# Optimization experiments

Measured on AMD Instinct MI355X. Metric: run time of the kernel, lower is better.

## Reference

```python
import jax, jax.numpy as jnp
import numpy as np

P = 7          # corr_size (patch size)
PAD = P // 2   # displacement radius
PP = P * P     # 49 correlation channels
CHANS = [512, 1024, 512, 256, 256, 256]
HW = [64, 32, 16, 8, 4, 2]
B = 8


def _spatial_correlation(f1, f2):
    """out[b, pi*P+pj, y, x] = sum_c f1[b,c,y,x] * f2[b,c,y+pi-PAD, x+pj-PAD] (zero pad)."""
    Bb, C, H, W = f1.shape
    f2p = jnp.pad(f2, ((0, 0), (0, 0), (PAD, PAD), (PAD, PAD)))
    outs = [jnp.sum(f1 * f2p[:, :, di:di + H, dj:dj + W], axis=1)
            for di in range(P) for dj in range(P)]
    return jnp.stack(outs, axis=1)  # [B, P*P, H, W]


def _corr_lstm_cell(feat, feat_pre, h_pre, c_pre, w, b):
    corr = jax.nn.leaky_relu(_spatial_correlation(feat, feat_pre), 0.01)  # [B,49,H,W]
    lstm_in = jnp.concatenate([corr, h_pre], axis=1)                      # [B,98,H,W]
    conv = jax.lax.conv_general_dilated(
        lstm_in, w, window_strides=(1, 1), padding='SAME',
        dimension_numbers=('NCHW', 'OIHW', 'NCHW')) + b[None, :, None, None]
    cc_i, cc_f, cc_o, cc_g = jnp.split(conv, 4, axis=1)
    i = jax.nn.sigmoid(cc_i)
    f = jax.nn.sigmoid(cc_f)
    o = jax.nn.sigmoid(cc_o)
    g = jnp.tanh(cc_g)
    c_next = f * c_pre + i * g
    h_next = o * jnp.tanh(c_next)
    return h_next, c_next, corr


def setup_inputs() -> dict:
    key = jax.random.key(0)
    ks = jax.random.split(key, 6 * 6)
    d = {}
    ki = 0
    for l in range(6):
        C, S = CHANS[l], HW[l]
        d[f'x{l}'] = 0.05 * jax.random.normal(ks[ki], (B, C, S, S), jnp.float32); ki += 1
        d[f'xp{l}'] = 0.05 * jax.random.normal(ks[ki], (B, C, S, S), jnp.float32); ki += 1
        d[f'h{l}'] = 0.1 * jax.random.normal(ks[ki], (B, PP, S, S), jnp.float32); ki += 1
        d[f'c{l}'] = 0.1 * jax.random.normal(ks[ki], (B, PP, S, S), jnp.float32); ki += 1
        fan_in = 2 * PP * 9
        lim = float(np.sqrt(6.0 / (fan_in + 4 * PP * 9)))
        d[f'w{l}'] = jax.random.uniform(ks[ki], (4 * PP, 2 * PP, 3, 3), jnp.float32, -lim, lim); ki += 1
        bias = jnp.zeros((4 * PP,), jnp.float32).at[PP:2 * PP].set(1.0)  # forget-gate bias = 1
        d[f'b{l}'] = bias; ki += 1
    return d


def reference(x0, x1, x2, x3, x4, x5,
              xp0, xp1, xp2, xp3, xp4, xp5,
              h0, h1, h2, h3, h4, h5,
              c0, c1, c2, c3, c4, c5,
              w0, w1, w2, w3, w4, w5,
              b0, b1, b2, b3, b4, b5):
    xs = [x0, x1, x2, x3, x4, x5]
    xps = [xp0, xp1, xp2, xp3, xp4, xp5]
    hs = [h0, h1, h2, h3, h4, h5]
    cs = [c0, c1, c2, c3, c4, c5]
    ws = [w0, w1, w2, w3, w4, w5]
    bs = [b0, b1, b2, b3, b4, b5]
    outs = []
    for l in range(6):
        outs.append(_corr_lstm_cell(xs[l], xps[l], hs[l], cs[l], ws[l], bs[l]))
    h_next = tuple(o[0] for o in outs)
    c_next = tuple(o[1] for o in outs)
    corrs = tuple(o[2] for o in outs)
    return h_next + c_next + corrs  # flat 18-tuple
```

## Files before the change

### kernel.cpp

```cpp
#include <hip/hip_runtime.h>
#include <stdint.h>

#define DEV __device__ __forceinline__

typedef _Float16 half2_t __attribute__((ext_vector_type(2)));
typedef _Float16 half4_t __attribute__((ext_vector_type(4)));
typedef __bf16   bf16x8  __attribute__((ext_vector_type(8)));
typedef float    floatx4 __attribute__((ext_vector_type(4)));
typedef float    floatx2 __attribute__((ext_vector_type(2)));

DEV float fdot2f(half2_t a, half2_t b, float c) {
#if __has_builtin(__builtin_amdgcn_fdot2)
  return __builtin_amdgcn_fdot2(a, b, c, false);
#else
  return c + (float)a[0] * (float)b[0] + (float)a[1] * (float)b[1];
#endif
}

DEV uint32_t f2bf(float f) {
  uint32_t u = __float_as_uint(f);
  return (u + 0x7FFFu + ((u >> 16) & 1u)) >> 16;
}

DEV half2_t mkh2(float a, float b) {
  half2_t r; r[0] = (_Float16)a; r[1] = (_Float16)b; return r;
}

struct CorrCfg {
  const float* gx[6]; const float* gxp[6];
  int wg_start[3];
  int small_start[3];
  int S[3], C[3], tiles_x[3], tiles_pb[3], cpl[3];
  int sS[3], sC[3];
  long long poff[3], spoff[3];
};

template<int TH, int TWD>
__global__ __launch_bounds__(128)
void corr_kernel(CorrCfg cfg, float* __restrict__ partial)
{
  int wg = blockIdx.x;
  if (wg >= cfg.small_start[0]) {
    int lvl = (wg >= cfg.small_start[2]) ? 2 : (wg >= cfg.small_start[1]) ? 1 : 0;
    long long i = (long long)(wg - cfg.small_start[lvl])*128 + threadIdx.x;
    const int S = cfg.sS[lvl], C = cfg.sC[lvl], SS = S*S;
    if (i >= (long long)8*49*SS) return;
    const float* X  = cfg.gx[lvl+3];
    const float* XP = cfg.gxp[lvl+3];
    int xc_ = (int)(i % S); int yc = (int)((i/S) % S);
    int d = (int)((i/SS) % 49); int b = (int)(i/((long long)49*SS));
    int yy = yc + d/7 - 3, xx = xc_ + (d%7) - 3;
    float s = 0.f;
    if (yy >= 0 && yy < S && xx >= 0 && xx < S) {
      const float* xb = X  + (size_t)b*C*SS + (size_t)yc*S + xc_;
      const float* pb = XP + (size_t)b*C*SS + (size_t)yy*S + xx;
      #pragma unroll 4
      for (int c = 0; c < C; ++c) s += xb[(size_t)c*SS] * pb[(size_t)c*SS];
    }
    partial[cfg.spoff[lvl] + i] = s;
    return;
  }
  constexpr int NT  = 128;
  constexpr int HWC = TWD + 6;
  constexpr int ST  = TWD + 10;
  constexpr int NPOS = (TH+6)*HWC;
  constexpr int PER  = (NPOS + NT - 1)/NT;
  __shared__ half2_t ldsbuf[2][2][(TH+6)*ST] __attribute__((aligned(16)));

  int lvl = (wg >= cfg.wg_start[2]) ? 2 : (wg >= cfg.wg_start[1]) ? 1 : 0;
  wg -= cfg.wg_start[lvl];
  const float* X  = cfg.gx[lvl];
  const float* XP = cfg.gxp[lvl];
  const int S = cfg.S[lvl], C = cfg.C[lvl];
  const int txc = cfg.tiles_x[lvl], tpb = cfg.tiles_pb[lvl], cpl = cfg.cpl[lvl];
  const int per_split = 8 * tpb;
  const int sp = wg / per_split;
  const int rem = wg - sp*per_split;
  const int b = rem / tpb;
  const int t = rem - b*tpb;
  const int y0 = (t / txc) * TH, x0t = (t % txc) * TWD;
  const int tid = threadIdx.x;
  const int tx = tid & (TWD/2 - 1), ty = tid / (TWD/2);
  const int cbase = sp * cpl;
  const size_t SS = (size_t)S*S;
  const float* Xb  = X  + (size_t)b*C*SS;
  const float* XPb = XP + (size_t)b*C*SS;
  const int py = y0 + ty, px = x0t + 2*tx;
  const size_t qoff = (size_t)py*S + px;

  int  f_lds[PER]; int f_go[PER]; bool f_ok[PER], f_val[PER];
  #pragma unroll
  for (int s = 0; s < PER; ++s) {
    int i = tid + s*NT;
    int r = i / HWC, c = i - r*HWC;
    int gy = y0 + r - 3, gx = x0t + c - 3;
    bool val = (i < NPOS);
    bool ok = val && gy >= 0 && gy < S && gx >= 0 && gx < S;
    f_val[s] = val; f_ok[s] = ok;
    f_go[s] = ok ? gy*S + gx : 0;
    f_lds[s] = val ? r*ST + c : 0;
  }

  floatx2 acc[49];
  #pragma unroll
  for (int d = 0; d < 49; ++d) acc[d] = (floatx2)0.0f;

  float fl[2][PER][2];
  float xc[4][2], xn[4][2];

#define FILL_LOAD(c0v) { \
  _Pragma("unroll") for (int pr = 0; pr < 2; ++pr) { \
    const float* p0_ = XPb + (size_t)(cbase + (c0v) + 2*pr)*SS; \
    const float* p1_ = p0_ + SS; \
    _Pragma("unroll") for (int s = 0; s < PER; ++s) { \
      fl[pr][s][0] = f_ok[s] ? p0_[f_go[s]] : 0.f; \
      fl[pr][s][1] = f_ok[s] ? p1_[f_go[s]] : 0.f; } } }

#define XLOAD(dst, c0v) { \
  _Pragma("unroll") for (int c = 0; c < 4; ++c) { \
    const float* q_ = Xb + (size_t)(cbase + (c0v) + c)*SS + qoff; \
    dst[c][0] = q_[0]; dst[c][1] = q_[1]; } }

#define FILL_STORE(bbv) { \
  _Pragma("unroll") for (int pr = 0; pr < 2; ++pr) \
    _Pragma("unroll") for (int s = 0; s < PER; ++s) \
      if (f_val[s]) ldsbuf[bbv][pr][f_lds[s]] = mkh2(fl[pr][s][0], fl[pr][s][1]); }

#define COMPUTE(bbv) { \
  _Pragma("unroll") for (int pr = 0; pr < 2; ++pr) { \
    half2_t xq0 = mkh2(xc[2*pr][0], xc[2*pr+1][0]); \
    half2_t xq1 = mkh2(xc[2*pr][1], xc[2*pr+1][1]); \
    _Pragma("unroll") for (int di = 0; di < 7; ++di) { \
      const half2_t* row_ = &ldsbuf[bbv][pr][(ty+di)*ST + 2*tx]; \
      half2_t w_[8]; \
      _Pragma("unroll") for (int k = 0; k < 4; ++k) { \
        half4_t v_ = *(const half4_t*)(row_ + 2*k); \
        w_[2*k]   = __builtin_shufflevector(v_, v_, 0, 1); \
        w_[2*k+1] = __builtin_shufflevector(v_, v_, 2, 3); } \
      _Pragma("unroll") for (int dj = 0; dj < 7; ++dj) { \
        acc[di*7+dj].x = fdot2f(xq0, w_[dj],   acc[di*7+dj].x); \
        acc[di*7+dj].y = fdot2f(xq1, w_[dj+1], acc[di*7+dj].y); } } } }

  const int nchunk = cpl >> 2;
  FILL_LOAD(0); XLOAD(xc, 0);
  FILL_STORE(0);
  FILL_LOAD(4); XLOAD(xn, 4);
  __syncthreads();
  for (int k = 0; k < nchunk; ++k) {
    const int bb = k & 1;
    if (k+1 < nchunk) FILL_STORE(bb^1);
    if (k+2 < nchunk) FILL_LOAD((k+2)*4);
    COMPUTE(bb);
    #pragma unroll
    for (int c = 0; c < 4; ++c) { xc[c][0] = xn[c][0]; xc[c][1] = xn[c][1]; }
    if (k+2 < nchunk) XLOAD(xn, (k+2)*4);
    __syncthreads();
  }
#undef FILL_LOAD
#undef XLOAD
#undef FILL_STORE
#undef COMPUTE

  float* P = partial + cfg.poff[lvl] + ((size_t)sp*8 + b)*49*SS + qoff;
  #pragma unroll
  for (int d = 0; d < 49; ++d)
    *(floatx2*)(P + (size_t)d*SS) = acc[d];
}

__global__ __launch_bounds__(256)
void pack_w_kernel(const float* __restrict__ w0, const float* __restrict__ w1,
                   const float* __restrict__ w2, const float* __restrict__ w3,
                   const float* __restrict__ w4, const float* __restrict__ w5,
                   uint16_t* __restrict__ wpack)
{
  int idx = blockIdx.x*256 + threadIdx.x;
  int lvl = idx / 258048;
  int e = idx - lvl*258048;
  const float* W = lvl==0?w0:lvl==1?w1:lvl==2?w2:lvl==3?w3:lvl==4?w4:w5;
  int j = e & 7, lane = (e >> 3) & 63, rest = e >> 9;
  int s = rest % 36, tt = rest / 36;
  int n  = tt*16 + (lane & 15);
  int ch = (s & 3)*32 + (lane >> 4)*8 + j;
  int tap = s >> 2, ky = tap/3, kx = tap - 3*ky;
  float v = 0.f;
  if (n < 196 && ch < 98) v = W[((n*98 + ch)*3 + ky)*3 + kx];
  wpack[idx] = (uint16_t)f2bf(v);
}

struct P2Cfg {
  int blk_start[7];
  int S[6], nsplit[6];
  long long poff[6], lstm_off[6], corr_off[6];
  const float* h[6];
};
__global__ __launch_bounds__(256)
void pass2_kernel(P2Cfg cfg, const float* __restrict__ partial,
                  uint16_t* __restrict__ lstm, float* __restrict__ dout)
{
  int blk = blockIdx.x;
  int lvl = 0;
  while (lvl < 5 && blk >= cfg.blk_start[lvl+1]) ++lvl;
  long long i = (long long)(blk - cfg.blk_start[lvl])*256 + threadIdx.x;
  const int S = cfg.S[lvl], Sp = S + 2, SS = S*S;
  if (i >= (long long)8*98*SS) return;
  int pix = (int)(i % SS);
  int ch  = (int)((i / SS) % 98);
  int b   = (int)(i / ((long long)98*SS));
  float val;
  if (ch < 49) {
    const int nsp = cfg.nsplit[lvl];
    const float* P = partial + cfg.poff[lvl] + ((size_t)b*49 + ch)*SS + pix;
    const size_t spstride = (size_t)8*49*SS;
    float s = 0.f;
    for (int sp = 0; sp < nsp; ++sp) s += P[(size_t)sp*spstride];
    s = s < 0.f ? 0.01f*s : s;
    dout[cfg.corr_off[lvl] + ((size_t)b*49 + ch)*SS + pix] = s;
    val = s;
  } else {
    val = cfg.h[lvl][((size_t)b*49 + (ch - 49))*SS + pix];
  }
  int y = pix / S, x = pix - y*S;
  lstm[cfg.lstm_off[lvl] + ((size_t)(b*Sp + y + 1)*Sp + (x + 1))*128 + ch] =
      (uint16_t)f2bf(val);
}

struct CCfg {
  int wg_start[7];
  int S[6], tiles_x[6], tiles_pb[6], lwsh[6], mfc[6], mgrp[6];
  long long lstm_off[6], wp_off[6], conv_off[6];
};
__global__ __launch_bounds__(256)
void conv_kernel(CCfg cfg, const uint16_t* __restrict__ lstm,
                 const uint16_t* __restrict__ wpack, float* __restrict__ cout)
{
  int wg = blockIdx.x;
  int lvl = 0;
  while (lvl < 5 && wg >= cfg.wg_start[lvl+1]) ++lvl;
  wg -= cfg.wg_start[lvl];
  const int S = cfg.S[lvl], Sp = S + 2;
  const int lwsh = cfg.lwsh[lvl], msk = (1 << lwsh) - 1;
  const int tpb = cfg.tiles_pb[lvl];
  const int b = wg / tpb, t = wg - b*tpb;
  const int ty0 = (t / cfg.tiles_x[lvl]) << (6 - lwsh);
  const int tx0 = (t % cfg.tiles_x[lvl]) << lwsh;
  const int wave = threadIdx.x >> 6, lane = threadIdx.x & 63;
  const int nhalf = wave & 1, mhalf = wave >> 1;
  const int mfc = cfg.mfc[lvl];
  if (mhalf >= cfg.mgrp[lvl]) return;
  const int mi = lane & 15, q = lane >> 4;
  const int SS = S*S;
  const uint16_t* lb = lstm + cfg.lstm_off[lvl] + (size_t)b*Sp*Sp*128;
  int aoff[2];
  #pragma unroll
  for (int mf = 0; mf < 2; ++mf) {
    int p = mhalf*32 + mf*16 + mi;
    int pc = p < SS ? p : 0;
    int y = ty0 + (pc >> lwsh), xx = tx0 + (pc & msk);
    aoff[mf] = (y*Sp + xx)*128 + q*8;
  }
  const uint16_t* wb = wpack + cfg.wp_off[lvl]
                     + (size_t)(nhalf*7)*36*512 + (size_t)lane*8;
  floatx4 acc[2][7];
  #pragma unroll
  for (int mf = 0; mf < 2; ++mf)
    #pragma unroll
    for (int nt = 0; nt < 7; ++nt) acc[mf][nt] = (floatx4)0.0f;

#define CONV_LOAD(sv, AV, BV) { \
  int tap_ = (sv) >> 2, cs_ = (sv) & 3; \
  int ky_ = tap_ / 3, kx_ = tap_ - 3*ky_; \
  int ao_ = ((ky_*Sp + kx_) << 7) + (cs_ << 5); \
  _Pragma("unroll") for (int mf = 0; mf < 2; ++mf) \
    if (mf < mfc) AV[mf] = *(const bf16x8*)(lb + aoff[mf] + ao_); \
  _Pragma("unroll") for (int nt = 0; nt < 7; ++nt) \
    BV[nt] = *(const bf16x8*)(wb + (size_t)((nt)*36 + (sv))*512); }

#define CONV_MFMA(AV, BV) { \
  _Pragma("unroll") for (int nt = 0; nt < 7; ++nt) \
    _Pragma("unroll") for (int mf = 0; mf < 2; ++mf) \
      if (mf < mfc) acc[mf][nt] = __builtin_amdgcn_mfma_f32_16x16x32_bf16( \
                        AV[mf], BV[nt], acc[mf][nt], 0, 0, 0); }

  bf16x8 av0[2], bv0[7], av1[2], bv1[7];
  CONV_LOAD(0, av0, bv0);
  for (int s = 0; s < 36; s += 2) {
    CONV_LOAD(s+1, av1, bv1);
    CONV_MFMA(av0, bv0);
    if (s+2 < 36) CONV_LOAD(s+2, av0, bv0);
    CONV_MFMA(av1, bv1);
  }
#undef CONV_LOAD
#undef CONV_MFMA

  float* co = cout + cfg.conv_off[lvl] + (size_t)b*196*SS;
  #pragma unroll
  for (int mf = 0; mf < 2; ++mf) {
    if (mf < mfc) {
      #pragma unroll
      for (int nt = 0; nt < 7; ++nt) {
        const int n = nhalf*112 + nt*16 + mi;
        if (n < 196) {
          #pragma unroll
          for (int r = 0; r < 4; ++r) {
            const int p = mhalf*32 + mf*16 + q*4 + r;
            if (p < SS) {
              const int y = ty0 + (p >> lwsh), xx = tx0 + (p & msk);
              co[(size_t)n*SS + y*S + xx] = acc[mf][nt][r];
            }
          }
        }
      }
    }
  }
}

struct GCfg {
  int blk_start[7];
  int S[6];
  long long conv_off[6], h_off[6], c_off[6];
  const float* cpre[6]; const float* bias[6];
};
__global__ __launch_bounds__(256)
void gate_kernel(GCfg cfg, const float* __restrict__ convout, float* __restrict__ dout)
{
  int blk = blockIdx.x;
  int lvl = 0;
  while (lvl < 5 && blk >= cfg.blk_start[lvl+1]) ++lvl;
  long long e = (long long)(blk - cfg.blk_start[lvl])*256 + threadIdx.x;
  const int S = cfg.S[lvl];
  const int SS = S*S;
  if (e >= (long long)8*49*SS) return;
  int b = (int)(e / ((long long)49*SS));
  int r1 = (int)(e - (long long)b*49*SS);
  int ch = r1 / SS;
  int p  = r1 - ch*SS;
  const float* cv = convout + cfg.conv_off[lvl] + ((size_t)b*196 + ch)*SS + p;
  const float* bb = cfg.bias[lvl];
  float ci  = cv[0]              + bb[ch];
  float cf  = cv[(size_t)49*SS]  + bb[ch+49];
  float co_ = cv[(size_t)98*SS]  + bb[ch+98];
  float cg  = cv[(size_t)147*SS] + bb[ch+147];
  float ig = 1.f/(1.f + __expf(-ci));
  float fg = 1.f/(1.f + __expf(-cf));
  float og = 1.f/(1.f + __expf(-co_));
  float g  = 1.f - 2.f/(__expf(2.f*cg) + 1.f);
  float cp = cfg.cpre[lvl][e];
  float cn = fg*cp + ig*g;
  float hn = og * (1.f - 2.f/(__expf(2.f*cn) + 1.f));
  dout[cfg.h_off[lvl] + e] = hn;
  dout[cfg.c_off[lvl] + e] = cn;
}

extern "C" void kernel_launch(void* const* d_in, const int* in_sizes, int n_in,
                              void* d_out, int out_size, void* d_ws, size_t ws_size,
                              hipStream_t stream)
{
  const float *x[6], *xp[6], *h[6], *cpre[6], *w[6], *bias[6];
  for (int l = 0; l < 6; ++l) {
    x[l]    = (const float*)d_in[6*l + 0];
    xp[l]   = (const float*)d_in[6*l + 1];
    h[l]    = (const float*)d_in[6*l + 2];
    cpre[l] = (const float*)d_in[6*l + 3];
    w[l]    = (const float*)d_in[6*l + 4];
    bias[l] = (const float*)d_in[6*l + 5];
  }
  static const int SL[6] = {64,32,16,8,4,2};
  static const int CL[6] = {512,1024,512,256,256,256};
  int NSPL[6] = {8,16,16,1,1,1};

  long long hsz[6], lstm_off[6], conv_off[6], h_off[6], poff[6];
  long long a1 = 0, a2 = 0, a3 = 0;
  for (int l = 0; l < 6; ++l) {
    int S = SL[l], Sp = S + 2;
    hsz[l] = 8LL*49*S*S;
    lstm_off[l] = a1; a1 += 8LL*Sp*Sp*128;
    conv_off[l] = a2; a2 += 8LL*196*S*S;
    h_off[l]    = a3; a3 += hsz[l];
  }
  long long pa = 0;
  for (int l = 0; l < 6; ++l) { poff[l] = pa; pa += (long long)NSPL[l]*hsz[l]; }
  {
    long long pr_bytes = (pa > a2 ? pa : a2) * 4;
    long long need = a1*2 + 6LL*258048*2 + pr_bytes;
    if (need > (long long)ws_size) {
      NSPL[0] = 4; NSPL[1] = 8; NSPL[2] = 16;
      pa = 0;
      for (int l = 0; l < 6; ++l) { poff[l] = pa; pa += (long long)NSPL[l]*hsz[l]; }
    }
  }
  const long long GRP = a3;
  const long long LSTM_ELEMS = a1;

  uint16_t* lstm  = (uint16_t*)d_ws;
  uint16_t* wpack = (uint16_t*)((char*)d_ws + LSTM_ELEMS*2);
  float* partial  = (float*)((char*)d_ws + LSTM_ELEMS*2 + 6LL*258048*2);
  float* convout  = partial;
  float* dout = (float*)d_out;

  {
    CorrCfg ccfg;
    static const int tpb[3] = {16, 4, 1};
    static const int txx[3] = {4, 2, 1};
    for (int l = 0; l < 6; ++l) { ccfg.gx[l] = x[l]; ccfg.gxp[l] = xp[l]; }
    int start = 0;
    for (int l = 0; l < 3; ++l) {
      ccfg.wg_start[l] = start;
      ccfg.S[l] = SL[l]; ccfg.C[l] = CL[l];
      ccfg.tiles_x[l] = txx[l]; ccfg.tiles_pb[l] = tpb[l];
      ccfg.cpl[l] = CL[l]/NSPL[l];
      ccfg.poff[l] = poff[l];
      start += NSPL[l]*8*tpb[l];
    }
    for (int l = 0; l < 3; ++l) {
      ccfg.small_start[l] = start;
      ccfg.sS[l] = SL[l+3]; ccfg.sC[l] = CL[l+3];
      ccfg.spoff[l] = poff[l+3];
      start += (int)((hsz[l+3] + 127)/128);
    }
    corr_kernel<16,16><<<start, 128, 0, stream>>>(ccfg, partial);
  }
  hipMemsetAsync(lstm, 0, (size_t)LSTM_ELEMS*2, stream);
  pack_w_kernel<<<6048, 256, 0, stream>>>(w[0],w[1],w[2],w[3],w[4],w[5], wpack);
  {
    P2Cfg p2; int start = 0;
    for (int l = 0; l < 6; ++l) {
      p2.blk_start[l] = start;
      start += (int)((8LL*98*SL[l]*SL[l] + 255)/256);
      p2.S[l] = SL[l]; p2.nsplit[l] = NSPL[l];
      p2.poff[l] = poff[l]; p2.lstm_off[l] = lstm_off[l];
      p2.corr_off[l] = 2*GRP + h_off[l];
      p2.h[l] = h[l];
    }
    p2.blk_start[6] = start;
    pass2_kernel<<<start, 256, 0, stream>>>(p2, partial, lstm, dout);
  }
  {
    CCfg cc;
    static const int ctpb[6] = {64, 16, 4, 1, 1, 1};
    static const int ctx[6]  = {4, 2, 1, 1, 1, 1};
    static const int clw[6]  = {4, 4, 4, 3, 2, 1};
    static const int cmfc[6] = {2, 2, 2, 2, 1, 1};
    static const int cmg[6]  = {2, 2, 2, 2, 1, 1};
    int start = 0;
    for (int l = 0; l < 6; ++l) {
      cc.wg_start[l] = start; start += 8*ctpb[l];
      cc.S[l] = SL[l]; cc.tiles_x[l] = ctx[l]; cc.tiles_pb[l] = ctpb[l];
      cc.lwsh[l] = clw[l]; cc.mfc[l] = cmfc[l]; cc.mgrp[l] = cmg[l];
      cc.lstm_off[l] = lstm_off[l];
      cc.wp_off[l] = 258048LL*l;
      cc.conv_off[l] = conv_off[l];
    }
    cc.wg_start[6] = start;
    conv_kernel<<<start, 256, 0, stream>>>(cc, lstm, wpack, convout);
  }
  {
    GCfg gc; int start = 0;
    for (int l = 0; l < 6; ++l) {
      gc.blk_start[l] = start;
      start += (int)((hsz[l] + 255)/256);
      gc.S[l] = SL[l];
      gc.conv_off[l] = conv_off[l];
      gc.h_off[l] = h_off[l];
      gc.c_off[l] = GRP + h_off[l];
      gc.cpre[l] = cpre[l];
      gc.bias[l] = bias[l];
    }
    gc.blk_start[6] = start;
    gate_kernel<<<start, 256, 0, stream>>>(gc, convout, dout);
  }
  (void)in_sizes; (void)n_in; (void)out_size; (void)ws_size;
}
```

Measured before the change: 530.2 us.

## Store fp16 partials, vectorize corr loads, and tile pass2 through LDS

Split-channel correlation partials are now written as fp16 instead of fp32, which halves partial traffic between the corr kernel and pass2. The corr kernel's halo fill now uses float4 global loads with packed fp16 conversion (cvt_pkrtz), and the X loads use float2. pass2 is restructured to gather a group of pixels into LDS and then write the channel-last bf16 LSTM input as packed 32-bit pairs, so the scattered 16-bit writes become coalesced ones. Rounding partial sums to fp16 before reduction adds precision loss, and the float4 halo load needs 16-byte alignment for the tile columns.

```diff
diff --git a/kernel.cpp b/kernel.cpp
--- a/kernel.cpp
+++ b/kernel.cpp
@@ -17,13 +17,17 @@
 #endif
 }
 
+DEV half2_t pkh2(float a, float b) {
+#if __has_builtin(__builtin_amdgcn_cvt_pkrtz)
+  return __builtin_bit_cast(half2_t, __builtin_amdgcn_cvt_pkrtz(a, b));
+#else
+  half2_t r; r[0] = (_Float16)a; r[1] = (_Float16)b; return r;
+#endif
+}
+
 DEV uint32_t f2bf(float f) {
   uint32_t u = __float_as_uint(f);
   return (u + 0x7FFFu + ((u >> 16) & 1u)) >> 16;
-}
-
-DEV half2_t mkh2(float a, float b) {
-  half2_t r; r[0] = (_Float16)a; r[1] = (_Float16)b; return r;
 }
 
 struct CorrCfg {
@@ -37,7 +41,7 @@
 
 template<int TH, int TWD>
 __global__ __launch_bounds__(128)
-void corr_kernel(CorrCfg cfg, float* __restrict__ partial)
+void corr_kernel(CorrCfg cfg, _Float16* __restrict__ partial)
 {
   int wg = blockIdx.x;
   if (wg >= cfg.small_start[0]) {
@@ -54,18 +58,19 @@
     if (yy >= 0 && yy < S && xx >= 0 && xx < S) {
       const float* xb = X  + (size_t)b*C*SS + (size_t)yc*S + xc_;
       const float* pb = XP + (size_t)b*C*SS + (size_t)yy*S + xx;
-      #pragma unroll 4
+      #pragma unroll 8
       for (int c = 0; c < C; ++c) s += xb[(size_t)c*SS] * pb[(size_t)c*SS];
     }
-    partial[cfg.spoff[lvl] + i] = s;
+    partial[cfg.spoff[lvl] + i] = (_Float16)s;
     return;
   }
   constexpr int NT  = 128;
-  constexpr int HWC = TWD + 6;
-  constexpr int ST  = TWD + 10;
-  constexpr int NPOS = (TH+6)*HWC;
-  constexpr int PER  = (NPOS + NT - 1)/NT;
-  __shared__ half2_t ldsbuf[2][2][(TH+6)*ST] __attribute__((aligned(16)));
+  constexpr int ROWS = TH + 6;
+  constexpr int COLS = TWD + 6;
+  constexpr int ST   = TWD + 10;
+  constexpr int SLOTS = ROWS * 6 * 2;
+  constexpr int PER   = (SLOTS + NT - 1)/NT;
+  __shared__ half2_t ldsbuf[2][2][ROWS*ST] __attribute__((aligned(16)));
 
   int lvl = (wg >= cfg.wg_start[2]) ? 2 : (wg >= cfg.wg_start[1]) ? 1 : 0;
   wg -= cfg.wg_start[lvl];
@@ -88,48 +93,55 @@
   const int py = y0 + ty, px = x0t + 2*tx;
   const size_t qoff = (size_t)py*S + px;
 
-  int  f_lds[PER]; int f_go[PER]; bool f_ok[PER], f_val[PER];
+  int f_go[PER], f_base[PER], f_col0[PER], f_pr[PER];
+  bool f_ok[PER], f_val[PER];
   #pragma unroll
   for (int s = 0; s < PER; ++s) {
     int i = tid + s*NT;
-    int r = i / HWC, c = i - r*HWC;
-    int gy = y0 + r - 3, gx = x0t + c - 3;
-    bool val = (i < NPOS);
-    bool ok = val && gy >= 0 && gy < S && gx >= 0 && gx < S;
-    f_val[s] = val; f_ok[s] = ok;
-    f_go[s] = ok ? gy*S + gx : 0;
-    f_lds[s] = val ? r*ST + c : 0;
+    bool val = (i < SLOTS);
+    int ii = val ? i : 0;
+    int pr = ii & 1;
+    int rest = ii >> 1;
+    int q = rest % 6;
+    int r = rest / 6;
+    int gy = y0 + r - 3;
+    int gx0 = x0t - 4 + 4*q;
+    bool ok = val && gy >= 0 && gy < S && gx0 >= 0 && (gx0 + 3) < S;
+    f_val[s] = val; f_ok[s] = ok; f_pr[s] = pr;
+    f_go[s] = ok ? gy*S + gx0 : 0;
+    f_col0[s] = 4*q - 1;
+    f_base[s] = r*ST;
   }
 
   floatx2 acc[49];
   #pragma unroll
   for (int d = 0; d < 49; ++d) acc[d] = (floatx2)0.0f;
 
-  float fl[2][PER][2];
-  float xc[4][2], xn[4][2];
+  floatx4 fl[PER][2];
+  floatx2 xc[4], xn[4];
 
 #define FILL_LOAD(c0v) { \
-  _Pragma("unroll") for (int pr = 0; pr < 2; ++pr) { \
-    const float* p0_ = XPb + (size_t)(cbase + (c0v) + 2*pr)*SS; \
-    const float* p1_ = p0_ + SS; \
-    _Pragma("unroll") for (int s = 0; s < PER; ++s) { \
-      fl[pr][s][0] = f_ok[s] ? p0_[f_go[s]] : 0.f; \
-      fl[pr][s][1] = f_ok[s] ? p1_[f_go[s]] : 0.f; } } }
+  _Pragma("unroll") for (int s = 0; s < PER; ++s) { \
+    const float* p_ = XPb + (size_t)(cbase + (c0v) + 2*f_pr[s])*SS + f_go[s]; \
+    if (f_ok[s]) { fl[s][0] = *(const floatx4*)p_; fl[s][1] = *(const floatx4*)(p_ + SS); } \
+    else { fl[s][0] = (floatx4)0.f; fl[s][1] = (floatx4)0.f; } } }
 
 #define XLOAD(dst, c0v) { \
-  _Pragma("unroll") for (int c = 0; c < 4; ++c) { \
-    const float* q_ = Xb + (size_t)(cbase + (c0v) + c)*SS + qoff; \
-    dst[c][0] = q_[0]; dst[c][1] = q_[1]; } }
+  _Pragma("unroll") for (int c = 0; c < 4; ++c) \
+    dst[c] = *(const floatx2*)(Xb + (size_t)(cbase + (c0v) + c)*SS + qoff); }
 
 #define FILL_STORE(bbv) { \
-  _Pragma("unroll") for (int pr = 0; pr < 2; ++pr) \
-    _Pragma("unroll") for (int s = 0; s < PER; ++s) \
-      if (f_val[s]) ldsbuf[bbv][pr][f_lds[s]] = mkh2(fl[pr][s][0], fl[pr][s][1]); }
+  _Pragma("unroll") for (int s = 0; s < PER; ++s) if (f_val[s]) { \
+    half2_t* plane_ = &ldsbuf[bbv][f_pr[s]][0]; \
+    _Pragma("unroll") for (int j = 0; j < 4; ++j) { \
+      int col_ = f_col0[s] + j; \
+      if (col_ >= 0 && col_ < COLS) \
+        plane_[f_base[s] + col_] = pkh2(fl[s][0][j], fl[s][1][j]); } } }
 
 #define COMPUTE(bbv) { \
   _Pragma("unroll") for (int pr = 0; pr < 2; ++pr) { \
-    half2_t xq0 = mkh2(xc[2*pr][0], xc[2*pr+1][0]); \
-    half2_t xq1 = mkh2(xc[2*pr][1], xc[2*pr+1][1]); \
+    half2_t xq0 = pkh2(xc[2*pr].x, xc[2*pr+1].x); \
+    half2_t xq1 = pkh2(xc[2*pr].y, xc[2*pr+1].y); \
     _Pragma("unroll") for (int di = 0; di < 7; ++di) { \
       const half2_t* row_ = &ldsbuf[bbv][pr][(ty+di)*ST + 2*tx]; \
       half2_t w_[8]; \
@@ -152,7 +164,7 @@
     if (k+2 < nchunk) FILL_LOAD((k+2)*4);
     COMPUTE(bb);
     #pragma unroll
-    for (int c = 0; c < 4; ++c) { xc[c][0] = xn[c][0]; xc[c][1] = xn[c][1]; }
+    for (int c = 0; c < 4; ++c) xc[c] = xn[c];
     if (k+2 < nchunk) XLOAD(xn, (k+2)*4);
     __syncthreads();
   }
@@ -161,10 +173,12 @@
 #undef FILL_STORE
 #undef COMPUTE
 
-  float* P = partial + cfg.poff[lvl] + ((size_t)sp*8 + b)*49*SS + qoff;
+  _Float16* P = partial + cfg.poff[lvl] + ((size_t)sp*8 + b)*49*SS + qoff;
   #pragma unroll
-  for (int d = 0; d < 49; ++d)
-    *(floatx2*)(P + (size_t)d*SS) = acc[d];
+  for (int d = 0; d < 49; ++d) {
+    half2_t pk = pkh2(acc[d].x, acc[d].y);
+    *(uint32_t*)(P + (size_t)d*SS) = *(const uint32_t*)&pk;
+  }
 }
 
 __global__ __launch_bounds__(256)
@@ -189,39 +203,54 @@
 
 struct P2Cfg {
   int blk_start[7];
-  int S[6], nsplit[6];
+  int S[6], nsplit[6], pxg[6], lg[6], gpb[6];
   long long poff[6], lstm_off[6], corr_off[6];
   const float* h[6];
 };
 __global__ __launch_bounds__(256)
-void pass2_kernel(P2Cfg cfg, const float* __restrict__ partial,
-                  uint16_t* __restrict__ lstm, float* __restrict__ dout)
+void pass2_kernel(P2Cfg cfg, const _Float16* __restrict__ partial,
+                  uint32_t* __restrict__ lstm, float* __restrict__ dout)
 {
+  __shared__ float lds[64*99];
   int blk = blockIdx.x;
   int lvl = 0;
   while (lvl < 5 && blk >= cfg.blk_start[lvl+1]) ++lvl;
-  long long i = (long long)(blk - cfg.blk_start[lvl])*256 + threadIdx.x;
+  int rel = blk - cfg.blk_start[lvl];
   const int S = cfg.S[lvl], Sp = S + 2, SS = S*S;
-  if (i >= (long long)8*98*SS) return;
-  int pix = (int)(i % SS);
-  int ch  = (int)((i / SS) % 98);
-  int b   = (int)(i / ((long long)98*SS));
-  float val;
-  if (ch < 49) {
-    const int nsp = cfg.nsplit[lvl];
-    const float* P = partial + cfg.poff[lvl] + ((size_t)b*49 + ch)*SS + pix;
-    const size_t spstride = (size_t)8*49*SS;
-    float s = 0.f;
-    for (int sp = 0; sp < nsp; ++sp) s += P[(size_t)sp*spstride];
-    s = s < 0.f ? 0.01f*s : s;
-    dout[cfg.corr_off[lvl] + ((size_t)b*49 + ch)*SS + pix] = s;
-    val = s;
-  } else {
-    val = cfg.h[lvl][((size_t)b*49 + (ch - 49))*SS + pix];
-  }
-  int y = pix / S, x = pix - y*S;
-  lstm[cfg.lstm_off[lvl] + ((size_t)(b*Sp + y + 1)*Sp + (x + 1))*128 + ch] =
-      (uint16_t)f2bf(val);
+  const int PXG = cfg.pxg[lvl], lg = cfg.lg[lvl], gpb = cfg.gpb[lvl];
+  const int b = rel / gpb, g = rel - b*gpb;
+  const int pixbase = g * PXG;
+  const int tid = threadIdx.x;
+  const int nsp = cfg.nsplit[lvl];
+  const size_t spstride = (size_t)8*49*SS;
+  for (int e = tid; e < PXG*98; e += 256) {
+    int pxl = e & (PXG-1);
+    int ch  = e >> lg;
+    int pix = pixbase + pxl;
+    float v;
+    if (ch < 49) {
+      const _Float16* P = partial + cfg.poff[lvl] + ((size_t)b*49 + ch)*SS + pix;
+      float s = 0.f;
+      for (int sp = 0; sp < nsp; ++sp) s += (float)P[(size_t)sp*spstride];
+      s = s < 0.f ? 0.01f*s : s;
+      dout[cfg.corr_off[lvl] + ((size_t)b*49 + ch)*SS + pix] = s;
+      v = s;
+    } else {
+      v = cfg.h[lvl][((size_t)b*49 + (ch - 49))*SS + pix];
+    }
+    lds[pxl*99 + ch] = v;
+  }
+  __syncthreads();
+  uint32_t* Lb = lstm + (cfg.lstm_off[lvl] >> 1);
+  for (int f = tid; f < (PXG << 6); f += 256) {
+    int pxl = f >> 6, c2 = f & 63;
+    int pix = pixbase + pxl;
+    int y = pix / S, x = pix - y*S;
+    int c0 = 2*c2, c1 = c0 + 1;
+    float v0 = c0 < 98 ? lds[pxl*99 + c0] : 0.f;
+    float v1 = c1 < 98 ? lds[pxl*99 + c1] : 0.f;
+    Lb[((size_t)(b*Sp + y + 1)*Sp + (x + 1))*64 + c2] = f2bf(v0) | (f2bf(v1) << 16);
+  }
 }
 
 struct CCfg {
@@ -380,7 +409,7 @@
   long long pa = 0;
   for (int l = 0; l < 6; ++l) { poff[l] = pa; pa += (long long)NSPL[l]*hsz[l]; }
   {
-    long long pr_bytes = (pa > a2 ? pa : a2) * 4;
+    long long pr_bytes = (pa*2 > a2*4 ? pa*2 : a2*4);
     long long need = a1*2 + 6LL*258048*2 + pr_bytes;
     if (need > (long long)ws_size) {
       NSPL[0] = 4; NSPL[1] = 8; NSPL[2] = 16;
@@ -393,8 +422,8 @@
 
   uint16_t* lstm  = (uint16_t*)d_ws;
   uint16_t* wpack = (uint16_t*)((char*)d_ws + LSTM_ELEMS*2);
-  float* partial  = (float*)((char*)d_ws + LSTM_ELEMS*2 + 6LL*258048*2);
-  float* convout  = partial;
+  _Float16* partial = (_Float16*)((char*)d_ws + LSTM_ELEMS*2 + 6LL*258048*2);
+  float* convout  = (float*)partial;
   float* dout = (float*)d_out;
 
   {
@@ -419,20 +448,25 @@
     }
     corr_kernel<16,16><<<start, 128, 0, stream>>>(ccfg, partial);
   }
-  hipMemsetAsync(lstm, 0, (size_t)LSTM_ELEMS*2, stream);
+  (void)hipMemsetAsync(lstm, 0, (size_t)LSTM_ELEMS*2, stream);
   pack_w_kernel<<<6048, 256, 0, stream>>>(w[0],w[1],w[2],w[3],w[4],w[5], wpack);
   {
     P2Cfg p2; int start = 0;
+    static const int PXGL[6] = {64,64,64,64,16,4};
+    static const int LGL[6]  = {6,6,6,6,4,2};
     for (int l = 0; l < 6; ++l) {
       p2.blk_start[l] = start;
-      start += (int)((8LL*98*SL[l]*SL[l] + 255)/256);
+      int gpb = (SL[l]*SL[l]) / PXGL[l]; if (gpb < 1) gpb = 1;
+      p2.gpb[l] = gpb;
+      start += 8 * gpb;
       p2.S[l] = SL[l]; p2.nsplit[l] = NSPL[l];
+      p2.pxg[l] = PXGL[l]; p2.lg[l] = LGL[l];
       p2.poff[l] = poff[l]; p2.lstm_off[l] = lstm_off[l];
       p2.corr_off[l] = 2*GRP + h_off[l];
       p2.h[l] = h[l];
     }
     p2.blk_start[6] = start;
-    pass2_kernel<<<start, 256, 0, stream>>>(p2, partial, lstm, dout);
+    pass2_kernel<<<start, 256, 0, stream>>>(p2, partial, (uint32_t*)lstm, dout);
   }
   {
     CCfg cc;
```

Result: faster. 503.4 us (-5.1%).
